# Kernel optimization log

Hardware: AMD Instinct MI355X
Metric: run time of the kernel (lower is better)

## Reference

```python
import jax, jax.numpy as jnp
import numpy as np

B, H, Wd, CIN = 4, 64, 64, 65   # batch, height, width, in_channels (incl. time)
COUT = 256                      # out_channels (incl. time)
K = 3
KK = K * K
PAD, STRIDE = 1, 1
SOUT = 4                        # output_stabilizer_size (C4 rotations)
CURV = 1.0                      # Lorentz manifold curvature k
LIN_FEAT = (CIN - 1) * KK + 1   # 577


def make_c4_z2_indices(ksize):
    # (out_rotation, in_stabilizer=1, u, v, [s, u_src, v_src]) index table,
    # realizing the C4 filter rotation as a gather (as in GrouPy).
    f = np.arange(ksize * ksize).reshape(ksize, ksize)
    inds = np.zeros((4, 1, ksize, ksize, 3), dtype=np.int64)
    for r in range(4):
        rot = np.rot90(f, r)
        u, v = np.unravel_index(rot, (ksize, ksize))
        inds[r, 0, :, :, 1] = u
        inds[r, 0, :, :, 2] = v
    return inds

INDS = make_c4_z2_indices(K)


def setup_inputs() -> dict:
    key = jax.random.key(0)
    k1, k2, k3 = jax.random.split(key, 3)
    stdv = float(np.sqrt(2.0 / ((CIN - 1) * KK)))  # reset_parameters
    x = jax.random.normal(k1, (B, H, Wd, CIN), dtype=jnp.float32)
    W = jax.random.uniform(k2, (COUT, LIN_FEAT), minval=-stdv, maxval=stdv, dtype=jnp.float32)
    b = jax.random.uniform(k3, (COUT,), minval=-stdv, maxval=stdv, dtype=jnp.float32)
    return {"x": x, "W": W, "b": b}


def _unfold(x):
    # x: (B, C, H, W) -> (B, C*KK, Ho*Wo) in torch.nn.Unfold layout (channel-major, kernel-minor)
    xp = jnp.pad(x, ((0, 0), (0, 0), (PAD, PAD), (PAD, PAD)))
    ho = (H + 2 * PAD - K) // STRIDE + 1
    wo = (Wd + 2 * PAD - K) // STRIDE + 1
    cols = [xp[:, :, i:i + ho * STRIDE:STRIDE, j:j + wo * STRIDE:STRIDE]
            for i in range(K) for j in range(K)]
    p = jnp.stack(cols, axis=2)  # (B, C, KK, ho, wo)
    return p.reshape(B, CIN * KK, ho * wo), ho, wo


def _forward(x, W, b):
    # torch code does x.view(B, C, H, W) on channel-last data: a reshape, not a permute.
    xv = x.reshape(B, CIN, H, Wd)
    patches, ho, wo = _unfold(xv)
    patches = jnp.transpose(patches, (0, 2, 1))          # (B, P, C*KK)
    P = patches.shape[1]
    patches = patches.reshape(B, P, CIN, 1, K, K)
    patches = jnp.broadcast_to(patches, (B, P, CIN, SOUT, K, K))  # repeat over group dim
    # --- group-equivariant filter transform realized as a gather on patches ---
    ir = INDS.reshape(-1, 3)                              # (SOUT*KK, 3)
    pi = patches[:, :, :, ir[:, 0], ir[:, 1], ir[:, 2]]   # (B, P, C, SOUT*KK)
    pi = pi.reshape(B, P, CIN, SOUT, KK)
    pt = jnp.transpose(pi, (3, 0, 1, 2, 4)).reshape(SOUT, B, P, CIN * KK)
    # --- extract_lorentz_patches (vectorized over group dim) ---
    sqrt_k = jnp.sqrt(jnp.float32(CURV))
    t = jnp.maximum(pt[..., :KK], sqrt_k)                 # clamp time components
    t_resc = jnp.sqrt(jnp.sum(t * t, axis=-1, keepdims=True) - (KK - 1) * CURV)
    sp = pt[..., KK:]                                     # (SOUT,B,P,(C-1)*KK) channel-major
    sp = sp.reshape(SOUT, B, P, CIN - 1, KK).swapaxes(-1, -2).reshape(SOUT, B, P, (CIN - 1) * KK)
    pre = jnp.concatenate([t_resc, sp], axis=-1)          # (SOUT,B,P,LIN_FEAT)
    # --- LorentzFullyConnected: linear, then recompute time from space norm ---
    y = jnp.einsum('gbpf,of->gbpo', pre, W) + b           # (SOUT,B,P,COUT)
    y_sp = y[..., 1:]
    y_t = jnp.sqrt(jnp.sum(y_sp * y_sp, axis=-1, keepdims=True) + CURV)
    out = jnp.concatenate([y_t, y_sp], axis=-1)
    out = jnp.transpose(out, (1, 0, 2, 3)).reshape(B, SOUT, ho, wo, COUT)
    return out


def reference(x, W, b):
    return _forward(x, W, b)
```

## Files before the change

### kernel.cpp

```cpp
#include <hip/hip_runtime.h>
#include <hip/hip_bf16.h>

#define CIN 65
#define LIN 577
#define NSTEP 18
#define M_  16384

typedef __bf16 bf16x8 __attribute__((ext_vector_type(8)));
typedef float  f32x4  __attribute__((ext_vector_type(4)));
typedef unsigned short u16x8 __attribute__((ext_vector_type(8)));

__constant__ int SIG[4][9] = {
  {0,1,2,3,4,5,6,7,8},
  {2,5,8,1,4,7,0,3,6},
  {8,7,6,5,4,3,2,1,0},
  {6,3,0,7,4,1,8,5,2}};

__device__ __forceinline__ int swzm(int r) { return (r ^ (r >> 2)) & 3; }

__global__ void prep_w(const float* __restrict__ W, __hip_bfloat16* __restrict__ Wg,
                       float* __restrict__ W0c) {
  int idx = blockIdx.x * 256 + threadIdx.x;
  if (idx < 4 * NSTEP * 8192) {
    int e   = idx & 7;
    int jc  = (idx >> 3) & 3;
    int col = (idx >> 5) & 255;
    int ks  = (idx >> 13) % NSTEP;
    int g   = idx / (NSTEP * 8192);
    int lc  = jc ^ swzm(col);
    int m   = ks >> 1;
    int c1  = (ks & 1) * 32 + lc * 8 + e;
    int k   = SIG[(4 - g) & 3][m];
    Wg[idx] = __float2bfloat16(W[col * LIN + 1 + k * 64 + c1]);
  } else {
    int j = idx - 4 * NSTEP * 8192;
    if (j < 256) W0c[j] = W[j * LIN];
  }
}

__global__ __launch_bounds__(512) void im2col_k(const float* __restrict__ x,
                                                __hip_bfloat16* __restrict__ A,
                                                float* __restrict__ T) {
  __shared__ float lds[CIN * 3 * 72];
  const int b = blockIdx.x >> 6, py = blockIdx.x & 63;
  const int tid = threadIdx.x;
  const float* xb = x + (size_t)b * (CIN * 4096);

  for (int i = tid; i < CIN * 3 * 18; i += 512)
    *(f32x4*)&lds[i * 4] = (f32x4){0.f, 0.f, 0.f, 0.f};
  __syncthreads();
  for (int i = tid; i < CIN * 3 * 16; i += 512) {
    int pr = i >> 4, j = i & 15;
    int c = pr / 3, dy = pr - c * 3;
    int hy = py + dy - 1;
    if (hy >= 0 && hy < 64)
      *(f32x4*)&lds[c * 216 + dy * 72 + 4 + j * 4] =
          *(const f32x4*)(xb + c * 4096 + hy * 64 + j * 4);
  }
  __syncthreads();

  const int wave = tid >> 6, px = tid & 63;
  const int rowid = (blockIdx.x << 6) | px;
  const int rb2 = rowid >> 8, krow = rowid & 255;
#pragma unroll
  for (int qi = 0; qi < 9; ++qi) {
    int q = wave * 9 + qi;
    int m = q >> 3, cb8 = q & 7;
    int ks = m * 2 + (cb8 >> 2);
    int jc = (cb8 & 3) ^ swzm(krow);
    int dy = m / 3, dx = m - dy * 3;
    const float* src = &lds[(1 + cb8 * 8) * 216 + dy * 72 + 3 + dx + px];
    u16x8 pk;
#pragma unroll
    for (int e = 0; e < 8; ++e) {
      union { __hip_bfloat16 h; unsigned short u; } cv;
      cv.h = __float2bfloat16(src[e * 216]);
      pk[e] = cv.u;
    }
    *(u16x8*)(A + ((((size_t)(rb2 * NSTEP + ks) << 8 | krow) << 2 | jc) << 3)) = pk;
  }
  if (wave == 0) {
    float s = 0.f;
#pragma unroll
    for (int m = 0; m < 9; ++m) {
      float t = fmaxf(lds[(m / 3) * 72 + 3 + (m % 3) + px], 1.f);
      s += t * t;
    }
    T[rowid] = sqrtf(s - 8.f);
  }
}

__device__ __forceinline__ void async_cp16(const void* g, void* ldsbase) {
  __builtin_amdgcn_global_load_lds(
      (const __attribute__((address_space(1))) void*)g,
      (__attribute__((address_space(3))) void*)ldsbase, 16, 0, 0);
}

__global__ __launch_bounds__(512, 2) void gemm_k(const __hip_bfloat16* __restrict__ A,
                                                 const __hip_bfloat16* __restrict__ Wg,
                                                 const float* __restrict__ bias,
                                                 const float* __restrict__ W0c,
                                                 const float* __restrict__ T,
                                                 float* __restrict__ out) {
  __shared__ __align__(16) char smem[65536];
  const int tid = threadIdx.x, wave = tid >> 6, lane = tid & 63;
  const int fr = lane & 15, fq = lane >> 4;
  const int rb2 = blockIdx.x, g = blockIdx.y;
  const int brow = rb2 << 8;
  const int wr = (wave >> 2) * 128, wcb = (wave & 3) * 64;
  const __hip_bfloat16* Asrc0 = A  + ((size_t)(rb2 * NSTEP) << 13);
  const __hip_bfloat16* Bsrc0 = Wg + ((size_t)(g   * NSTEP) << 13);
  f32x4 acc[8][4] = {};

  auto STAGE = [&](int buf, int ks) {
#pragma unroll
    for (int h = 0; h < 2; ++h) {
      async_cp16(Asrc0 + (ks << 13) + (h * 512 + tid) * 8,
                 smem + buf * 16384 + (h * 512 + wave * 64) * 16);
      async_cp16(Bsrc0 + (ks << 13) + (h * 512 + tid) * 8,
                 smem + 32768 + buf * 16384 + (h * 512 + wave * 64) * 16);
    }
  };
  auto COMPUTE = [&](int buf) {
    const char* Ab = smem + buf * 16384;
    const char* Bb = smem + 32768 + buf * 16384;
    bf16x8 af[8], bf[4];
#pragma unroll
    for (int i = 0; i < 8; ++i) {
      int r = wr + i * 16 + fr;
      af[i] = *(const bf16x8*)(Ab + r * 64 + ((fq ^ swzm(r)) << 4));
    }
#pragma unroll
    for (int j = 0; j < 4; ++j) {
      int c = wcb + j * 16 + fr;
      bf[j] = *(const bf16x8*)(Bb + c * 64 + ((fq ^ swzm(c)) << 4));
    }
#pragma unroll
    for (int i = 0; i < 8; ++i)
#pragma unroll
      for (int j = 0; j < 4; ++j)
        acc[i][j] = __builtin_amdgcn_mfma_f32_16x16x32_bf16(af[i], bf[j], acc[i][j], 0, 0, 0);
  };

  STAGE(0, 0);
  __syncthreads();
  int cur = 0;
  for (int ks = 0; ks < NSTEP - 1; ++ks) {
    STAGE(cur ^ 1, ks + 1);
    COMPUTE(cur);
    __syncthreads();
    cur ^= 1;
  }
  float* Tsh = (float*)(smem + 4096);
  if (tid < 256) Tsh[tid] = T[brow + tid];
  COMPUTE(cur);
  __syncthreads();

  float* Ps = (float*)smem;
  float bo[4], w0v[4]; int oc[4];
#pragma unroll
  for (int j = 0; j < 4; ++j) {
    oc[j]  = wcb + j * 16 + fr;
    bo[j]  = bias[oc[j]];
    w0v[j] = W0c[oc[j]];
  }
#pragma unroll
  for (int i = 0; i < 8; ++i) {
#pragma unroll
    for (int rr = 0; rr < 4; ++rr) {
      int rl = wr + i * 16 + fq * 4 + rr;
      int row = brow + rl;
      size_t obase = ((size_t)(((row >> 12) * 4 + g) * 4096 + (row & 4095)) << 8);
      float tval = Tsh[rl];
      float s = 0.f;
#pragma unroll
      for (int j = 0; j < 4; ++j) {
        float y = acc[i][j][rr] + bo[j] + tval * w0v[j];
        if (oc[j] != 0) { s += y * y; out[obase + oc[j]] = y; }
      }
      s += __shfl_xor(s, 1); s += __shfl_xor(s, 2);
      s += __shfl_xor(s, 4); s += __shfl_xor(s, 8);
      if (fr == 0) Ps[rl * 4 + (wave & 3)] = s;
    }
  }
  __syncthreads();
  if (tid < 256) {
    int row = brow + tid;
    float s = Ps[tid * 4] + Ps[tid * 4 + 1] + Ps[tid * 4 + 2] + Ps[tid * 4 + 3] + 1.0f;
    out[(size_t)(((row >> 12) * 4 + g) * 4096 + (row & 4095)) << 8] = sqrtf(s);
  }
}

extern "C" void kernel_launch(void* const* d_in, const int* in_sizes, int n_in,
                              void* d_out, int out_size, void* d_ws, size_t ws_size,
                              hipStream_t stream) {
  const float* x    = (const float*)d_in[0];
  const float* W    = (const float*)d_in[1];
  const float* bias = (const float*)d_in[2];
  float* out = (float*)d_out;

  char* ws = (char*)d_ws;
  __hip_bfloat16* Wg  = (__hip_bfloat16*)ws;
  float*          W0c = (float*)(ws + 1179648);
  float*          T   = (float*)(ws + 1180672);
  __hip_bfloat16* A   = (__hip_bfloat16*)(ws + 1246208);

  prep_w  <<<2306, 256, 0, stream>>>(W, Wg, W0c);
  im2col_k<<<256, 512, 0, stream>>>(x, A, T);
  gemm_k  <<<dim3(64, 4), 512, 0, stream>>>(A, Wg, bias, W0c, T, out);
}
```

Before: 51.19 us.

## Merge weight prep into im2col kernel and halve GEMM row tile

Folds the weight-conversion work into the im2col launch as extra blocks, which drops one kernel launch, and has it write 8 contiguous bf16 values per thread. The im2col output moves to a simple chunk-major layout, with the swizzle now applied at GEMM staging time. The GEMM tile shrinks from 256 to 128 rows, giving 512 blocks at occupancy 4 and less shared memory, and the block index is remapped for L2 locality. The time weight column is read directly from W. The trade-off is more blocks each reloading B tiles, and less per-block reuse of those tiles.

Measured after the change: 44.53 us. 1.15x faster.

```diff
diff --git a/kernel.cpp b/kernel.cpp
--- a/kernel.cpp
+++ b/kernel.cpp
@@ -18,34 +18,33 @@
 
 __device__ __forceinline__ int swzm(int r) { return (r ^ (r >> 2)) & 3; }
 
-__global__ void prep_w(const float* __restrict__ W, __hip_bfloat16* __restrict__ Wg,
-                       float* __restrict__ W0c) {
-  int idx = blockIdx.x * 256 + threadIdx.x;
-  if (idx < 4 * NSTEP * 8192) {
-    int e   = idx & 7;
-    int jc  = (idx >> 3) & 3;
-    int col = (idx >> 5) & 255;
-    int ks  = (idx >> 13) % NSTEP;
-    int g   = idx / (NSTEP * 8192);
-    int lc  = jc ^ swzm(col);
-    int m   = ks >> 1;
-    int c1  = (ks & 1) * 32 + lc * 8 + e;
-    int k   = SIG[(4 - g) & 3][m];
-    Wg[idx] = __float2bfloat16(W[col * LIN + 1 + k * 64 + c1]);
-  } else {
-    int j = idx - 4 * NSTEP * 8192;
-    if (j < 256) W0c[j] = W[j * LIN];
-  }
-}
-
-__global__ __launch_bounds__(512) void im2col_k(const float* __restrict__ x,
-                                                __hip_bfloat16* __restrict__ A,
-                                                float* __restrict__ T) {
+__global__ __launch_bounds__(512) void prep_k(const float* __restrict__ x,
+                                              const float* __restrict__ W,
+                                              __hip_bfloat16* __restrict__ A,
+                                              __hip_bfloat16* __restrict__ Wg,
+                                              float* __restrict__ T) {
   __shared__ float lds[CIN * 3 * 72];
+  const int tid = threadIdx.x;
+  if (blockIdx.x >= 256) {
+    int pidx = (blockIdx.x - 256) * 512 + tid;
+    int jc  = pidx & 3;
+    int col = (pidx >> 2) & 255;
+    int t   = pidx >> 10;
+    int ks  = t % NSTEP, g = t / NSTEP;
+    int k   = SIG[(4 - g) & 3][ks >> 1];
+    const float* src = W + col * LIN + 1 + k * 64 + (ks & 1) * 32 + jc * 8;
+    u16x8 pk;
+#pragma unroll
+    for (int e = 0; e < 8; ++e) {
+      union { __hip_bfloat16 h; unsigned short u; } cv;
+      cv.h = __float2bfloat16(src[e]);
+      pk[e] = cv.u;
+    }
+    *(u16x8*)(Wg + (size_t)pidx * 8) = pk;
+    return;
+  }
   const int b = blockIdx.x >> 6, py = blockIdx.x & 63;
-  const int tid = threadIdx.x;
   const float* xb = x + (size_t)b * (CIN * 4096);
-
   for (int i = tid; i < CIN * 3 * 18; i += 512)
     *(f32x4*)&lds[i * 4] = (f32x4){0.f, 0.f, 0.f, 0.f};
   __syncthreads();
@@ -61,13 +60,10 @@
 
   const int wave = tid >> 6, px = tid & 63;
   const int rowid = (blockIdx.x << 6) | px;
-  const int rb2 = rowid >> 8, krow = rowid & 255;
 #pragma unroll
   for (int qi = 0; qi < 9; ++qi) {
     int q = wave * 9 + qi;
     int m = q >> 3, cb8 = q & 7;
-    int ks = m * 2 + (cb8 >> 2);
-    int jc = (cb8 & 3) ^ swzm(krow);
     int dy = m / 3, dx = m - dy * 3;
     const float* src = &lds[(1 + cb8 * 8) * 216 + dy * 72 + 3 + dx + px];
     u16x8 pk;
@@ -77,7 +73,7 @@
       cv.h = __float2bfloat16(src[e * 216]);
       pk[e] = cv.u;
     }
-    *(u16x8*)(A + ((((size_t)(rb2 * NSTEP + ks) << 8 | krow) << 2 | jc) << 3)) = pk;
+    *(u16x8*)(A + ((size_t)q * M_ + rowid) * 8) = pk;
   }
   if (wave == 0) {
     float s = 0.f;
@@ -96,37 +92,44 @@
       (__attribute__((address_space(3))) void*)ldsbase, 16, 0, 0);
 }
 
-__global__ __launch_bounds__(512, 2) void gemm_k(const __hip_bfloat16* __restrict__ A,
+__global__ __launch_bounds__(512, 4) void gemm_k(const __hip_bfloat16* __restrict__ A,
                                                  const __hip_bfloat16* __restrict__ Wg,
+                                                 const float* __restrict__ W,
                                                  const float* __restrict__ bias,
-                                                 const float* __restrict__ W0c,
                                                  const float* __restrict__ T,
                                                  float* __restrict__ out) {
-  __shared__ __align__(16) char smem[65536];
+  __shared__ __align__(16) char smem[49152];
+  const int fid = blockIdx.x;
+  const int lid = ((fid & 7) << 6) | (fid >> 3);
+  const int g = lid & 3, rb = lid >> 2;
+  const int brow = rb << 7;
   const int tid = threadIdx.x, wave = tid >> 6, lane = tid & 63;
   const int fr = lane & 15, fq = lane >> 4;
-  const int rb2 = blockIdx.x, g = blockIdx.y;
-  const int brow = rb2 << 8;
-  const int wr = (wave >> 2) * 128, wcb = (wave & 3) * 64;
-  const __hip_bfloat16* Asrc0 = A  + ((size_t)(rb2 * NSTEP) << 13);
-  const __hip_bfloat16* Bsrc0 = Wg + ((size_t)(g   * NSTEP) << 13);
-  f32x4 acc[8][4] = {};
+  const int wr = (wave >> 2) * 64, wcb = (wave & 3) * 64;
+
+  const int arow = tid >> 2;
+  const int alc  = (tid & 3) ^ swzm(arow);
+  const int bcol0 = tid >> 2;
+  const int blc0  = (tid & 3) ^ swzm(bcol0);
+  const int bcol1 = 128 + (tid >> 2);
+  const int blc1  = (tid & 3) ^ swzm(bcol1);
+  f32x4 acc[4][4] = {};
 
   auto STAGE = [&](int buf, int ks) {
-#pragma unroll
-    for (int h = 0; h < 2; ++h) {
-      async_cp16(Asrc0 + (ks << 13) + (h * 512 + tid) * 8,
-                 smem + buf * 16384 + (h * 512 + wave * 64) * 16);
-      async_cp16(Bsrc0 + (ks << 13) + (h * 512 + tid) * 8,
-                 smem + 32768 + buf * 16384 + (h * 512 + wave * 64) * 16);
-    }
+    int qb = (ks >> 1) * 8 + (ks & 1) * 4;
+    async_cp16(A + (((size_t)(qb + alc) * M_ + brow + arow) << 3),
+               smem + buf * 8192 + wave * 1024);
+    const __hip_bfloat16* bs = Wg + ((size_t)(g * NSTEP + ks) << 13);
+    char* bl = smem + 16384 + buf * 16384 + wave * 1024;
+    async_cp16(bs + bcol0 * 32 + blc0 * 8, bl);
+    async_cp16(bs + bcol1 * 32 + blc1 * 8, bl + 8192);
   };
   auto COMPUTE = [&](int buf) {
-    const char* Ab = smem + buf * 16384;
-    const char* Bb = smem + 32768 + buf * 16384;
-    bf16x8 af[8], bf[4];
-#pragma unroll
-    for (int i = 0; i < 8; ++i) {
+    const char* Ab = smem + buf * 8192;
+    const char* Bb = smem + 16384 + buf * 16384;
+    bf16x8 af[4], bf[4];
+#pragma unroll
+    for (int i = 0; i < 4; ++i) {
       int r = wr + i * 16 + fr;
       af[i] = *(const bf16x8*)(Ab + r * 64 + ((fq ^ swzm(r)) << 4));
     }
@@ -136,7 +139,7 @@
       bf[j] = *(const bf16x8*)(Bb + c * 64 + ((fq ^ swzm(c)) << 4));
     }
 #pragma unroll
-    for (int i = 0; i < 8; ++i)
+    for (int i = 0; i < 4; ++i)
 #pragma unroll
       for (int j = 0; j < 4; ++j)
         acc[i][j] = __builtin_amdgcn_mfma_f32_16x16x32_bf16(af[i], bf[j], acc[i][j], 0, 0, 0);
@@ -151,21 +154,21 @@
     __syncthreads();
     cur ^= 1;
   }
-  float* Tsh = (float*)(smem + 4096);
-  if (tid < 256) Tsh[tid] = T[brow + tid];
+  float* Tsh = (float*)smem;
+  float* Ps  = (float*)(smem + 512);
+  if (tid < 128) Tsh[tid] = T[brow + tid];
   COMPUTE(cur);
   __syncthreads();
 
-  float* Ps = (float*)smem;
   float bo[4], w0v[4]; int oc[4];
 #pragma unroll
   for (int j = 0; j < 4; ++j) {
     oc[j]  = wcb + j * 16 + fr;
     bo[j]  = bias[oc[j]];
-    w0v[j] = W0c[oc[j]];
-  }
-#pragma unroll
-  for (int i = 0; i < 8; ++i) {
+    w0v[j] = W[oc[j] * LIN];
+  }
+#pragma unroll
+  for (int i = 0; i < 4; ++i) {
 #pragma unroll
     for (int rr = 0; rr < 4; ++rr) {
       int rl = wr + i * 16 + fq * 4 + rr;
@@ -184,7 +187,7 @@
     }
   }
   __syncthreads();
-  if (tid < 256) {
+  if (tid < 128) {
     int row = brow + tid;
     float s = Ps[tid * 4] + Ps[tid * 4 + 1] + Ps[tid * 4 + 2] + Ps[tid * 4 + 3] + 1.0f;
     out[(size_t)(((row >> 12) * 4 + g) * 4096 + (row & 4095)) << 8] = sqrtf(s);
@@ -200,12 +203,10 @@
   float* out = (float*)d_out;
 
   char* ws = (char*)d_ws;
-  __hip_bfloat16* Wg  = (__hip_bfloat16*)ws;
-  float*          W0c = (float*)(ws + 1179648);
-  float*          T   = (float*)(ws + 1180672);
-  __hip_bfloat16* A   = (__hip_bfloat16*)(ws + 1246208);
-
-  prep_w  <<<2306, 256, 0, stream>>>(W, Wg, W0c);
-  im2col_k<<<256, 512, 0, stream>>>(x, A, T);
-  gemm_k  <<<dim3(64, 4), 512, 0, stream>>>(A, Wg, bias, W0c, T, out);
-}
+  __hip_bfloat16* Wg = (__hip_bfloat16*)ws;
+  float*          T  = (float*)(ws + 1179648);
+  __hip_bfloat16* A  = (__hip_bfloat16*)(ws + 1245184);
+
+  prep_k<<<400, 512, 0, stream>>>(x, W, A, Wg, T);
+  gemm_k<<<512, 512, 0, stream>>>(A, Wg, W, bias, T, out);
+}
```
